# Performance work log

Hardware: AMD Instinct MI355X
Metric: run time of the kernel (lower is better)

Reference implementation:

```python
import jax, jax.numpy as jnp
import numpy as np

NEG_SLOPE = 0.2
LN_EPS = 1e-6

B, L, D, H = 32, 512, 256, 4
N = B * L
E = 65536
C = D  # per-head out channels (GATConv out_channels=d_model)


def setup_inputs() -> dict:
    key = jax.random.key(0)
    ks = jax.random.split(key, 10)
    s = 1.0 / np.sqrt(D)
    inputs = jax.random.normal(ks[0], (B, L, D), dtype=jnp.float32)
    edge_index = jax.random.randint(ks[1], (2, E), 0, N, dtype=jnp.int64)
    return {
        "inputs": inputs,
        "edge_index": edge_index,
        "ln_gamma": jnp.ones((D,), jnp.float32),
        "ln_beta": jnp.zeros((D,), jnp.float32),
        "W1": jax.random.normal(ks[2], (D, D), jnp.float32) * s,   # linear_before_gnn
        "b1": jnp.zeros((D,), jnp.float32),
        "W_gat": jax.random.normal(ks[3], (H * C, D), jnp.float32) * s,  # GATConv.lin (no bias)
        "att_src": jax.random.normal(ks[4], (H, C), jnp.float32) * s,
        "att_dst": jax.random.normal(ks[5], (H, C), jnp.float32) * s,
        "bias_gat": jnp.zeros((C,), jnp.float32),  # concat=False -> size out_channels
        "W2": jax.random.normal(ks[6], (D, D), jnp.float32) * s,   # linear_after_gnn
        "b2": jnp.zeros((D,), jnp.float32),
    }


def _gat_conv(x, edge_index, W_gat, att_src, att_dst, bias_gat):
    # x: [N, D] -> project to [N, H, C]
    xh = (x @ W_gat.T).reshape(N, H, C)
    # add self loops (PyG default add_self_loops=True)
    loops = jnp.arange(N, dtype=edge_index.dtype)
    src = jnp.concatenate([edge_index[0], loops])  # message source j
    dst = jnp.concatenate([edge_index[1], loops])  # message target i
    # per-node attention logits [N, H]
    a_src = jnp.einsum("nhc,hc->nh", xh, att_src)
    a_dst = jnp.einsum("nhc,hc->nh", xh, att_dst)
    # per-edge logits and segment softmax over destination node
    e = jax.nn.leaky_relu(a_src[src] + a_dst[dst], NEG_SLOPE)  # [Etot, H]
    e_max = jax.ops.segment_max(e, dst, num_segments=N)        # every node has a self loop
    e = jnp.exp(e - e_max[dst])
    denom = jax.ops.segment_sum(e, dst, num_segments=N)
    alpha = e / denom[dst]                                     # [Etot, H]
    # weighted message aggregation (dropout on alpha skipped: eval mode)
    msg = xh[src] * alpha[:, :, None]                          # [Etot, H, C]
    out = jax.ops.segment_sum(msg, dst, num_segments=N)        # [N, H, C]
    return out.mean(axis=1) + bias_gat                         # concat=False -> head mean


def reference(inputs, edge_index, ln_gamma, ln_beta, W1, b1, W_gat, att_src, att_dst, bias_gat, W2, b2):
    # LayerNorm(eps=1e-6)
    mu = inputs.mean(-1, keepdims=True)
    var = jnp.mean((inputs - mu) ** 2, axis=-1, keepdims=True)
    x = (inputs - mu) * jax.lax.rsqrt(var + LN_EPS) * ln_gamma + ln_beta
    x = x.reshape(-1, D)
    gnn_in = x @ W1.T + b1
    gnn_out = _gat_conv(gnn_in, edge_index, W_gat, att_src, att_dst, bias_gat)
    y = gnn_out @ W2.T + b2
    # dropout is identity in eval mode; residual add
    return y.reshape(B, L, D) + inputs
```

## Files before the change

### kernel.cpp

```cpp
#include <hip/hip_runtime.h>
#include <math.h>

#define N_NODES 16384
#define D_MODEL 256
#define H_HEADS 4
#define C_CH 256
#define E_EDGES 65536
#define ETOT (E_EDGES + N_NODES)
#define HC 1024

typedef __bf16 bf16x8 __attribute__((ext_vector_type(8)));
typedef __bf16 bf16x4 __attribute__((ext_vector_type(4)));
typedef float f32x4 __attribute__((ext_vector_type(4)));

__device__ __forceinline__ __bf16 f2bf(float f) { return (__bf16)f; }
__device__ __forceinline__ float bf2f(__bf16 b) { return (float)b; }

__global__ __launch_bounds__(256) void prep1_ln(
    const float* __restrict__ Wg, const float* __restrict__ att_src,
    const float* __restrict__ att_dst, const float* __restrict__ W2,
    const int* __restrict__ ei, const float* __restrict__ in,
    const float* __restrict__ gamma, const float* __restrict__ beta,
    float* __restrict__ t, float* __restrict__ V, int* __restrict__ deg,
    __bf16* __restrict__ x_ln)
{
    int b = blockIdx.x;
    int tid = threadIdx.x;
    if (b >= 640) {
        int wave = tid >> 6, lane = tid & 63;
        int row = (b - 640) * 4 + wave;
        float4 v = ((const float4*)(in + (size_t)row * D_MODEL))[lane];
        float s  = v.x + v.y + v.z + v.w;
        float sq = v.x*v.x + v.y*v.y + v.z*v.z + v.w*v.w;
        for (int off = 32; off; off >>= 1) {
            s  += __shfl_xor(s,  off);
            sq += __shfl_xor(sq, off);
        }
        float mean = s * (1.0f / D_MODEL);
        float var  = sq * (1.0f / D_MODEL) - mean * mean;
        float inv  = rsqrtf(var + 1e-6f);
        float4 g = ((const float4*)gamma)[lane];
        float4 bb = ((const float4*)beta)[lane];
        bf16x4 o;
        o[0] = f2bf((v.x - mean) * inv * g.x + bb.x);
        o[1] = f2bf((v.y - mean) * inv * g.y + bb.y);
        o[2] = f2bf((v.z - mean) * inv * g.z + bb.z);
        o[3] = f2bf((v.w - mean) * inv * g.w + bb.w);
        *(bf16x4*)(x_ln + (size_t)row * D_MODEL + lane * 4) = o;
        return;
    }
    if (b < 64) {
        int v = b >> 3, sl = b & 7, h = v & 3;
        const float* att = ((v < 4) ? att_src : att_dst) + h * C_CH;
        float acc = 0.f;
        #pragma unroll
        for (int j = 0; j < 32; ++j) {
            int c = sl * 32 + j;
            acc = fmaf(Wg[(size_t)(h * 256 + c) * 256 + tid], att[c], acc);
        }
        atomicAdd(&t[v * 256 + tid], acc);
    } else if (b < 320) {
        int bb = b - 64;
        int og = (bb & 63) * 4, h = bb >> 6;
        const float* w2r = W2 + (size_t)og * 256;
        const float* wgp = Wg + ((size_t)h * 256) * 256 + tid;
        float a0 = 0.f, a1 = 0.f, a2 = 0.f, a3 = 0.f;
        #pragma unroll 4
        for (int c = 0; c < 256; ++c) {
            float wv = wgp[(size_t)c * 256];
            a0 = fmaf(w2r[c],       wv, a0);
            a1 = fmaf(w2r[256 + c], wv, a1);
            a2 = fmaf(w2r[512 + c], wv, a2);
            a3 = fmaf(w2r[768 + c], wv, a3);
        }
        size_t base = (size_t)og * 1024 + h * 256 + tid;
        V[base]        = a0;
        V[base + 1024] = a1;
        V[base + 2048] = a2;
        V[base + 3072] = a3;
    } else {
        int e = (b - 320) * 256 + tid;
        int dst = (e < E_EDGES) ? ei[E_EDGES + e] : (e - E_EDGES);
        atomicAdd(deg + dst, 1);
    }
}

__global__ __launch_bounds__(256) void prep2(
    const float* __restrict__ t, const float* __restrict__ W1,
    const float* __restrict__ b1, const float* __restrict__ V,
    const float* __restrict__ W2, const float* __restrict__ bg,
    const float* __restrict__ b2, float* __restrict__ u2,
    float* __restrict__ c0, __bf16* __restrict__ Wz,
    float* __restrict__ bias_z, const int* __restrict__ deg,
    int* __restrict__ row_st)
{
    int b = blockIdx.x;
    int d = threadIdx.x;
    if (b < 64) {
        int v = b >> 3, sl = b & 7;
        const float* tv = t + v * 256;
        float acc = 0.f;
        #pragma unroll
        for (int j = 0; j < 32; ++j) {
            int k = sl * 32 + j;
            acc = fmaf(tv[k], W1[(size_t)k * 256 + d], acc);
        }
        atomicAdd(&u2[v * 256 + d], acc);
        if (d < 32) {
            float p = tv[sl * 32 + d] * b1[sl * 32 + d];
            for (int s = 16; s; s >>= 1) p += __shfl_xor(p, s);
            if (d == 0) atomicAdd(&c0[v], p);
        }
        return;
    }
    if (b == 320) {
        __shared__ int wsum[4];
        int lane = d & 63, wid = d >> 6;
        int base = d * 64;
        int run = 0;
        for (int j = 0; j < 64; ++j) run += deg[base + j];
        int x = run;
        #pragma unroll
        for (int off = 1; off < 64; off <<= 1) {
            int y = __shfl_up(x, off);
            if (lane >= off) x += y;
        }
        if (lane == 63) wsum[wid] = x;
        __syncthreads();
        int woff = 0;
        #pragma unroll
        for (int wdx = 0; wdx < 4; ++wdx)
            if (wdx < wid) woff += wsum[wdx];
        int excl = woff + x - run;
        int run2 = 0;
        for (int j = 0; j < 64; ++j) {
            row_st[base + j] = excl + run2;
            run2 += deg[base + j];
        }
        if (d == 255) row_st[N_NODES] = excl + run2;
        return;
    }
    int bb = b - 64;
    int og = (bb & 63) * 4, h = bb >> 6;
    int lane = d & 63, wid = d >> 6;
    const float* vr = V + (size_t)og * 1024 + h * 256;
    float a0 = 0.f, a1 = 0.f, a2 = 0.f, a3 = 0.f;
    #pragma unroll 4
    for (int k = 0; k < 256; ++k) {
        float w1v = W1[(size_t)k * 256 + d];
        a0 = fmaf(vr[k],        w1v, a0);
        a1 = fmaf(vr[1024 + k], w1v, a1);
        a2 = fmaf(vr[2048 + k], w1v, a2);
        a3 = fmaf(vr[3072 + k], w1v, a3);
    }
    size_t base = (size_t)og * 1024 + h * 256 + d;
    Wz[base]        = f2bf(a0);
    Wz[base + 1024] = f2bf(a1);
    Wz[base + 2048] = f2bf(a2);
    Wz[base + 3072] = f2bf(a3);

    __shared__ float red[4][4];
    float b1v = b1[d];
    #pragma unroll
    for (int j = 0; j < 4; ++j) {
        float p = vr[(size_t)j * 1024 + d] * b1v;
        for (int s = 32; s; s >>= 1) p += __shfl_xor(p, s);
        if (lane == 0) red[j][wid] = p;
    }
    __syncthreads();
    if (d < 4) {
        float s = red[d][0] + red[d][1] + red[d][2] + red[d][3];
        atomicAdd(&bias_z[og + d], 0.25f * s);
    }
    if (h == 0) {
        __syncthreads();
        float bgv = bg[d];
        #pragma unroll
        for (int j = 0; j < 4; ++j) {
            float q = W2[(size_t)(og + j) * 256 + d] * bgv;
            for (int s = 32; s; s >>= 1) q += __shfl_xor(q, s);
            if (lane == 0) red[j][wid] = q;
        }
        __syncthreads();
        if (d < 4) {
            float s = red[d][0] + red[d][1] + red[d][2] + red[d][3];
            atomicAdd(&bias_z[og + d], s + b2[og + d]);
        }
    }
}

__global__ __launch_bounds__(256) void logits_scatter(
    const __bf16* __restrict__ x_ln, const float* __restrict__ u2,
    const float* __restrict__ c0, float* __restrict__ a_src,
    float* __restrict__ a_dst, const int* __restrict__ ei,
    const int* __restrict__ row_st, int* __restrict__ cnt,
    int* __restrict__ csr_src)
{
    int b = blockIdx.x;
    int tid = threadIdx.x;
    if (b >= 4096) {
        int e = (b - 4096) * 256 + tid;
        int src, dst;
        if (e < E_EDGES) { src = ei[e]; dst = ei[E_EDGES + e]; }
        else             { src = dst = e - E_EDGES; }
        int pos = atomicAdd(cnt + dst, 1);
        csr_src[row_st[dst] + pos] = src;
        return;
    }
    __shared__ float u2s[8][256];
    __shared__ float c0s[8];
    #pragma unroll
    for (int k = 0; k < 8; ++k) u2s[k][tid] = u2[k * 256 + tid];
    if (tid < 8) c0s[tid] = c0[tid];
    __syncthreads();

    int wave = tid >> 6, lane = tid & 63;
    int n = b * 4 + wave;
    int v = lane >> 3, p = lane & 7;
    const __bf16* xp = x_ln + (size_t)n * D_MODEL + p * 32;
    const float*  up = &u2s[v][p * 32];
    float acc = 0.f;
    #pragma unroll
    for (int ti = 0; ti < 4; ++ti) {
        bf16x8 x = *(const bf16x8*)(xp + ti * 8);
        #pragma unroll
        for (int j = 0; j < 8; ++j)
            acc = fmaf(bf2f(x[j]), up[ti * 8 + j], acc);
    }
    acc += __shfl_xor(acc, 1);
    acc += __shfl_xor(acc, 2);
    acc += __shfl_xor(acc, 4);
    if (p == 0) {
        float o = acc + c0s[v];
        if (v < 4) a_src[n * H_HEADS + v] = o;
        else       a_dst[n * H_HEADS + (v - 4)] = o;
    }
}

__global__ __launch_bounds__(256) void gat_fused(
    const __bf16* __restrict__ x_ln, const float* __restrict__ a_src,
    const float* __restrict__ a_dst, const int* __restrict__ row_start,
    const int* __restrict__ csr_src, __bf16* __restrict__ agg)
{
    int wave = threadIdx.x >> 6, lane = threadIdx.x & 63;
    int i = blockIdx.x * 4 + wave;
    int rs = row_start[i], deg = row_start[i + 1] - rs;
    float4 ad = *(const float4*)(a_dst + i * H_HEADS);

    float acc[4][4] = {};
    float sm0 = 0.f, sm1 = 0.f, sm2 = 0.f, sm3 = 0.f;
    for (int e = 0; e < deg; ++e) {
        int s = csr_src[rs + e];
        float4 as = *(const float4*)(a_src + s * H_HEADS);
        float l0 = as.x + ad.x, l1 = as.y + ad.y, l2 = as.z + ad.z, l3 = as.w + ad.w;
        l0 = (l0 > 0.f) ? l0 : 0.2f * l0;
        l1 = (l1 > 0.f) ? l1 : 0.2f * l1;
        l2 = (l2 > 0.f) ? l2 : 0.2f * l2;
        l3 = (l3 > 0.f) ? l3 : 0.2f * l3;
        float w0 = __expf(l0), w1 = __expf(l1);
        float w2 = __expf(l2), w3 = __expf(l3);
        sm0 += w0; sm1 += w1; sm2 += w2; sm3 += w3;
        bf16x4 x = *(const bf16x4*)(x_ln + (size_t)s * D_MODEL + lane * 4);
        #pragma unroll
        for (int j = 0; j < 4; ++j) {
            float xv = bf2f(x[j]);
            acc[0][j] = fmaf(w0, xv, acc[0][j]);
            acc[1][j] = fmaf(w1, xv, acc[1][j]);
            acc[2][j] = fmaf(w2, xv, acc[2][j]);
            acc[3][j] = fmaf(w3, xv, acc[3][j]);
        }
    }
    float sc[4] = {0.25f / sm0, 0.25f / sm1, 0.25f / sm2, 0.25f / sm3};
    #pragma unroll
    for (int h = 0; h < 4; ++h) {
        bf16x4 o;
        #pragma unroll
        for (int j = 0; j < 4; ++j) o[j] = f2bf(acc[h][j] * sc[h]);
        *(bf16x4*)(agg + (size_t)i * HC + h * 256 + lane * 4) = o;
    }
}

#define APAD 72

__global__ __launch_bounds__(256) void gemm_skinny(
    const __bf16* __restrict__ A, const __bf16* __restrict__ B,
    const float* __restrict__ bias, const float* __restrict__ resid,
    float* __restrict__ outf, int K)
{
    __shared__ __align__(16) __bf16 As[64 * APAD];
    __shared__ __align__(16) __bf16 Bs[256 * APAD];
    int tid  = threadIdx.x;
    int lane = tid & 63;
    int w    = tid >> 6;
    int quad = lane >> 4;
    int l16  = lane & 15;
// ... 79 lines not shown
    for (int nt = 0; nt < 4; ++nt) {
        int col = n0 + nt * 16 + l16;
        float bv = bias[col];
        #pragma unroll
        for (int mt = 0; mt < 4; ++mt) {
            int row = m0 + mt * 16 + quad * 4;
            #pragma unroll
            for (int r = 0; r < 4; ++r) {
                size_t off = (size_t)(row + r) * C_CH + col;
                outf[off] = acc[mt][nt][r] + bv + resid[off];
            }
        }
    }
}

extern "C" void kernel_launch(void* const* d_in, const int* in_sizes, int n_in,
                              void* d_out, int out_size, void* d_ws, size_t ws_size,
                              hipStream_t stream)
{
    const float* inp      = (const float*)d_in[0];
    const int*   ei       = (const int*)  d_in[1];
    const float* ln_gamma = (const float*)d_in[2];
    const float* ln_beta  = (const float*)d_in[3];
    const float* W1       = (const float*)d_in[4];
    const float* b1       = (const float*)d_in[5];
    const float* W_gat    = (const float*)d_in[6];
    const float* att_src  = (const float*)d_in[7];
    const float* att_dst  = (const float*)d_in[8];
    const float* bias_gat = (const float*)d_in[9];
    const float* W2       = (const float*)d_in[10];
    const float* b2       = (const float*)d_in[11];

    char* ws = (char*)d_ws;
    __bf16* x_ln_bf   = (__bf16*)(ws);
    __bf16* agg_bf    = (__bf16*)(ws + (8ull  << 20));
    float*  V_f       = (float*)(ws + (40ull << 20));
    __bf16* Wz_b      = (__bf16*)(ws + (41ull << 20));
    float*  a_src_b   = (float*)(ws + (42ull << 20));
    float*  a_dst_b   = a_src_b + (size_t)N_NODES * H_HEADS;
    float*  t_vec     = a_dst_b + (size_t)N_NODES * H_HEADS;
    float*  u2        = t_vec + 8 * 256;
    float*  c0        = u2 + 8 * 256;
    float*  bias_z    = c0 + 8;
    int*    deg       = (int*)(bias_z + 256);
    int*    cnt       = deg + N_NODES;
    int*    row_st    = cnt + N_NODES;
    int*    csr_src   = row_st + N_NODES + 4;

    size_t zbytes = (8 * 256 + 8 * 256 + 8 + 256) * sizeof(float)
                  + 2 * N_NODES * sizeof(int);
    hipMemsetAsync(t_vec, 0, zbytes, stream);

    prep1_ln<<<640 + 4096, 256, 0, stream>>>(W_gat, att_src, att_dst, W2, ei,
                                             inp, ln_gamma, ln_beta,
                                             t_vec, V_f, deg, x_ln_bf);
    prep2<<<321, 256, 0, stream>>>(t_vec, W1, b1, V_f, W2, bias_gat, b2,
                                   u2, c0, Wz_b, bias_z, deg, row_st);
    logits_scatter<<<4096 + 320, 256, 0, stream>>>(x_ln_bf, u2, c0,
                                                   a_src_b, a_dst_b,
                                                   ei, row_st, cnt, csr_src);
    gat_fused<<<N_NODES / 4, 256, 0, stream>>>(x_ln_bf, a_src_b, a_dst_b,
                                               row_st, csr_src, agg_bf);
    gemm_skinny<<<N_NODES / 64, 256, 0, stream>>>(agg_bf, Wz_b, bias_z, inp,
                                                  (float*)d_out, HC);
}
```

Baseline: 181.8 us.

## Fuse LayerNorm into logits kernel and unroll GAT edge loop by two

LayerNorm moves out of the first prep kernel and into the logits/scatter kernel. The attention logits are now computed from the fp32 normalized values still in registers, so the bf16 x_ln no longer has to be re-read from memory. The per-node GAT aggregation loop is also unrolled by two edges so more gathers are in flight at once. The costs are higher register pressure in gat_fused and slightly different logits, because they now use fp32 instead of bf16-rounded inputs.

```diff
diff --git a/kernel.cpp b/kernel.cpp
--- a/kernel.cpp
+++ b/kernel.cpp
@@ -16,39 +16,14 @@
 __device__ __forceinline__ __bf16 f2bf(float f) { return (__bf16)f; }
 __device__ __forceinline__ float bf2f(__bf16 b) { return (float)b; }
 
-__global__ __launch_bounds__(256) void prep1_ln(
+__global__ __launch_bounds__(256) void prep_w(
     const float* __restrict__ Wg, const float* __restrict__ att_src,
     const float* __restrict__ att_dst, const float* __restrict__ W2,
-    const int* __restrict__ ei, const float* __restrict__ in,
-    const float* __restrict__ gamma, const float* __restrict__ beta,
-    float* __restrict__ t, float* __restrict__ V, int* __restrict__ deg,
-    __bf16* __restrict__ x_ln)
+    const int* __restrict__ ei,
+    float* __restrict__ t, float* __restrict__ V, int* __restrict__ deg)
 {
     int b = blockIdx.x;
     int tid = threadIdx.x;
-    if (b >= 640) {
-        int wave = tid >> 6, lane = tid & 63;
-        int row = (b - 640) * 4 + wave;
-        float4 v = ((const float4*)(in + (size_t)row * D_MODEL))[lane];
-        float s  = v.x + v.y + v.z + v.w;
-        float sq = v.x*v.x + v.y*v.y + v.z*v.z + v.w*v.w;
-        for (int off = 32; off; off >>= 1) {
-            s  += __shfl_xor(s,  off);
-            sq += __shfl_xor(sq, off);
-        }
-        float mean = s * (1.0f / D_MODEL);
-        float var  = sq * (1.0f / D_MODEL) - mean * mean;
-        float inv  = rsqrtf(var + 1e-6f);
-        float4 g = ((const float4*)gamma)[lane];
-        float4 bb = ((const float4*)beta)[lane];
-        bf16x4 o;
-        o[0] = f2bf((v.x - mean) * inv * g.x + bb.x);
-        o[1] = f2bf((v.y - mean) * inv * g.y + bb.y);
-        o[2] = f2bf((v.z - mean) * inv * g.z + bb.z);
-        o[3] = f2bf((v.w - mean) * inv * g.w + bb.w);
-        *(bf16x4*)(x_ln + (size_t)row * D_MODEL + lane * 4) = o;
-        return;
-    }
     if (b < 64) {
         int v = b >> 3, sl = b & 7, h = v & 3;
         const float* att = ((v < 4) ? att_src : att_dst) + h * C_CH;
@@ -189,12 +164,13 @@
     }
 }
 
-__global__ __launch_bounds__(256) void logits_scatter(
-    const __bf16* __restrict__ x_ln, const float* __restrict__ u2,
-    const float* __restrict__ c0, float* __restrict__ a_src,
-    float* __restrict__ a_dst, const int* __restrict__ ei,
-    const int* __restrict__ row_st, int* __restrict__ cnt,
-    int* __restrict__ csr_src)
+__global__ __launch_bounds__(256) void ln_logits_scatter(
+    const float* __restrict__ in, const float* __restrict__ gamma,
+    const float* __restrict__ beta, const float* __restrict__ u2,
+    const float* __restrict__ c0, __bf16* __restrict__ x_ln,
+    float* __restrict__ a_src, float* __restrict__ a_dst,
+    const int* __restrict__ ei, const int* __restrict__ row_st,
+    int* __restrict__ cnt, int* __restrict__ csr_src)
 {
     int b = blockIdx.x;
     int tid = threadIdx.x;
@@ -207,7 +183,7 @@
         csr_src[row_st[dst] + pos] = src;
         return;
     }
-    __shared__ float u2s[8][256];
+    __shared__ __align__(16) float u2s[8][256];
     __shared__ float c0s[8];
     #pragma unroll
     for (int k = 0; k < 8; ++k) u2s[k][tid] = u2[k * 256 + tid];
@@ -215,25 +191,38 @@
     __syncthreads();
 
     int wave = tid >> 6, lane = tid & 63;
-    int n = b * 4 + wave;
-    int v = lane >> 3, p = lane & 7;
-    const __bf16* xp = x_ln + (size_t)n * D_MODEL + p * 32;
-    const float*  up = &u2s[v][p * 32];
-    float acc = 0.f;
-    #pragma unroll
-    for (int ti = 0; ti < 4; ++ti) {
-        bf16x8 x = *(const bf16x8*)(xp + ti * 8);
-        #pragma unroll
-        for (int j = 0; j < 8; ++j)
-            acc = fmaf(bf2f(x[j]), up[ti * 8 + j], acc);
-    }
-    acc += __shfl_xor(acc, 1);
-    acc += __shfl_xor(acc, 2);
-    acc += __shfl_xor(acc, 4);
-    if (p == 0) {
-        float o = acc + c0s[v];
-        if (v < 4) a_src[n * H_HEADS + v] = o;
-        else       a_dst[n * H_HEADS + (v - 4)] = o;
+    int row = b * 4 + wave;
+    float4 v = ((const float4*)(in + (size_t)row * D_MODEL))[lane];
+    float s  = v.x + v.y + v.z + v.w;
+    float sq = v.x*v.x + v.y*v.y + v.z*v.z + v.w*v.w;
+    for (int off = 32; off; off >>= 1) {
+        s  += __shfl_xor(s,  off);
+        sq += __shfl_xor(sq, off);
+    }
+    float mean = s * (1.0f / D_MODEL);
+    float var  = sq * (1.0f / D_MODEL) - mean * mean;
+    float inv  = rsqrtf(var + 1e-6f);
+    float4 g  = ((const float4*)gamma)[lane];
+    float4 bb = ((const float4*)beta)[lane];
+    float xr0 = (v.x - mean) * inv * g.x + bb.x;
+    float xr1 = (v.y - mean) * inv * g.y + bb.y;
+    float xr2 = (v.z - mean) * inv * g.z + bb.z;
+    float xr3 = (v.w - mean) * inv * g.w + bb.w;
+    bf16x4 o;
+    o[0] = f2bf(xr0); o[1] = f2bf(xr1); o[2] = f2bf(xr2); o[3] = f2bf(xr3);
+    *(bf16x4*)(x_ln + (size_t)row * D_MODEL + lane * 4) = o;
+
+    #pragma unroll
+    for (int vv = 0; vv < 8; ++vv) {
+        float4 u = *(const float4*)&u2s[vv][lane * 4];
+        float p = xr0 * u.x + xr1 * u.y + xr2 * u.z + xr3 * u.w;
+        #pragma unroll
+        for (int off = 32; off; off >>= 1) p += __shfl_xor(p, off);
+        if (lane == 0) {
+            float oo = p + c0s[vv];
+            if (vv < 4) a_src[row * H_HEADS + vv] = oo;
+            else        a_dst[row * H_HEADS + (vv - 4)] = oo;
+        }
     }
 }
 
@@ -249,10 +238,52 @@
 
     float acc[4][4] = {};
     float sm0 = 0.f, sm1 = 0.f, sm2 = 0.f, sm3 = 0.f;
-    for (int e = 0; e < deg; ++e) {
+    int e = 0;
+    for (; e + 2 <= deg; e += 2) {
+        int s0 = csr_src[rs + e];
+        int s1 = csr_src[rs + e + 1];
+        float4 as0 = *(const float4*)(a_src + s0 * H_HEADS);
+        float4 as1 = *(const float4*)(a_src + s1 * H_HEADS);
+        bf16x4 x0 = *(const bf16x4*)(x_ln + (size_t)s0 * D_MODEL + lane * 4);
+        bf16x4 x1 = *(const bf16x4*)(x_ln + (size_t)s1 * D_MODEL + lane * 4);
+        float l00 = as0.x + ad.x, l01 = as0.y + ad.y,
+              l02 = as0.z + ad.z, l03 = as0.w + ad.w;
+        float l10 = as1.x + ad.x, l11 = as1.y + ad.y,
+              l12 = as1.z + ad.z, l13 = as1.w + ad.w;
+        l00 = (l00 > 0.f) ? l00 : 0.2f * l00;
+        l01 = (l01 > 0.f) ? l01 : 0.2f * l01;
+        l02 = (l02 > 0.f) ? l02 : 0.2f * l02;
+        l03 = (l03 > 0.f) ? l03 : 0.2f * l03;
+        l10 = (l10 > 0.f) ? l10 : 0.2f * l10;
+        l11 = (l11 > 0.f) ? l11 : 0.2f * l11;
+        l12 = (l12 > 0.f) ? l12 : 0.2f * l12;
+        l13 = (l13 > 0.f) ? l13 : 0.2f * l13;
+        float w00 = __expf(l00), w01 = __expf(l01),
+              w02 = __expf(l02), w03 = __expf(l03);
+        float w10 = __expf(l10), w11 = __expf(l11),
+              w12 = __expf(l12), w13 = __expf(l13);
+        sm0 += w00 + w10; sm1 += w01 + w11;
+        sm2 += w02 + w12; sm3 += w03 + w13;
+        #pragma unroll
+        for (int j = 0; j < 4; ++j) {
+            float xv0 = bf2f(x0[j]);
+            float xv1 = bf2f(x1[j]);
+            acc[0][j] = fmaf(w00, xv0, acc[0][j]);
+            acc[1][j] = fmaf(w01, xv0, acc[1][j]);
+            acc[2][j] = fmaf(w02, xv0, acc[2][j]);
+            acc[3][j] = fmaf(w03, xv0, acc[3][j]);
+            acc[0][j] = fmaf(w10, xv1, acc[0][j]);
+            acc[1][j] = fmaf(w11, xv1, acc[1][j]);
+            acc[2][j] = fmaf(w12, xv1, acc[2][j]);
+            acc[3][j] = fmaf(w13, xv1, acc[3][j]);
+        }
+    }
+    if (e < deg) {
         int s = csr_src[rs + e];
         float4 as = *(const float4*)(a_src + s * H_HEADS);
-        float l0 = as.x + ad.x, l1 = as.y + ad.y, l2 = as.z + ad.z, l3 = as.w + ad.w;
+        bf16x4 x = *(const bf16x4*)(x_ln + (size_t)s * D_MODEL + lane * 4);
+        float l0 = as.x + ad.x, l1 = as.y + ad.y,
+              l2 = as.z + ad.z, l3 = as.w + ad.w;
         l0 = (l0 > 0.f) ? l0 : 0.2f * l0;
         l1 = (l1 > 0.f) ? l1 : 0.2f * l1;
         l2 = (l2 > 0.f) ? l2 : 0.2f * l2;
@@ -260,7 +291,6 @@
         float w0 = __expf(l0), w1 = __expf(l1);
         float w2 = __expf(l2), w3 = __expf(l3);
         sm0 += w0; sm1 += w1; sm2 += w2; sm3 += w3;
-        bf16x4 x = *(const bf16x4*)(x_ln + (size_t)s * D_MODEL + lane * 4);
         #pragma unroll
         for (int j = 0; j < 4; ++j) {
             float xv = bf2f(x[j]);
@@ -425,14 +455,14 @@
                   + 2 * N_NODES * sizeof(int);
     hipMemsetAsync(t_vec, 0, zbytes, stream);
 
-    prep1_ln<<<640 + 4096, 256, 0, stream>>>(W_gat, att_src, att_dst, W2, ei,
-                                             inp, ln_gamma, ln_beta,
-                                             t_vec, V_f, deg, x_ln_bf);
+    prep_w<<<640, 256, 0, stream>>>(W_gat, att_src, att_dst, W2, ei,
+                                    t_vec, V_f, deg);
     prep2<<<321, 256, 0, stream>>>(t_vec, W1, b1, V_f, W2, bias_gat, b2,
                                    u2, c0, Wz_b, bias_z, deg, row_st);
-    logits_scatter<<<4096 + 320, 256, 0, stream>>>(x_ln_bf, u2, c0,
-                                                   a_src_b, a_dst_b,
-                                                   ei, row_st, cnt, csr_src);
+    ln_logits_scatter<<<4096 + 320, 256, 0, stream>>>(inp, ln_gamma, ln_beta,
+                                                      u2, c0, x_ln_bf,
+                                                      a_src_b, a_dst_b,
+                                                      ei, row_st, cnt, csr_src);
     gat_fused<<<N_NODES / 4, 256, 0, stream>>>(x_ln_bf, a_src_b, a_dst_b,
                                                row_st, csr_src, agg_bf);
     gemm_skinny<<<N_NODES / 64, 256, 0, stream>>>(agg_bf, Wz_b, bias_z, inp,
```

Result: no change. 184.2 us (+1.3%).

## Merge prep kernels, use fixed-slot adjacency buckets, unroll GAT edge loop

Applied to the files above, without the earlier changes.

Folds the two prep kernels into one launch. A single block now computes the attention-projected vectors and u2/c0 serially instead of through atomics, and the other blocks compute the fused W2·Wg·W1 weights through shared memory. The degree count and prefix scan are replaced by fixed-capacity per-node buckets of 64 slots filled by atomic counters. The GAT kernel loads each node's source list once per lane and shuffles it to every lane, with a 4-way unrolled edge loop that overlaps the gathers. This removes kernel launches and the serial scan, but silently assumes no node has an in-degree above 64, and the single-block prep step may become a serial tail.

```diff
diff --git a/kernel.cpp b/kernel.cpp
--- a/kernel.cpp
+++ b/kernel.cpp
@@ -8,6 +8,7 @@
 #define E_EDGES 65536
 #define ETOT (E_EDGES + N_NODES)
 #define HC 1024
+#define MAXDEG 64
 
 typedef __bf16 bf16x8 __attribute__((ext_vector_type(8)));
 typedef __bf16 bf16x4 __attribute__((ext_vector_type(4)));
@@ -16,19 +17,23 @@
 __device__ __forceinline__ __bf16 f2bf(float f) { return (__bf16)f; }
 __device__ __forceinline__ float bf2f(__bf16 b) { return (float)b; }
 
-__global__ __launch_bounds__(256) void prep1_ln(
+__global__ __launch_bounds__(256) void fused_prep_ln(
     const float* __restrict__ Wg, const float* __restrict__ att_src,
-    const float* __restrict__ att_dst, const float* __restrict__ W2,
+    const float* __restrict__ att_dst, const float* __restrict__ W1,
+    const float* __restrict__ b1, const float* __restrict__ W2,
+    const float* __restrict__ bg, const float* __restrict__ b2,
     const int* __restrict__ ei, const float* __restrict__ in,
     const float* __restrict__ gamma, const float* __restrict__ beta,
-    float* __restrict__ t, float* __restrict__ V, int* __restrict__ deg,
-    __bf16* __restrict__ x_ln)
+    __bf16* __restrict__ x_ln, __bf16* __restrict__ Wz,
+    float* __restrict__ bias_z, float* __restrict__ u2,
+    float* __restrict__ c0, int* __restrict__ cnt, int* __restrict__ csr)
 {
     int b = blockIdx.x;
     int tid = threadIdx.x;
-    if (b >= 640) {
+
+    if (b >= 577) {
         int wave = tid >> 6, lane = tid & 63;
-        int row = (b - 640) * 4 + wave;
+        int row = (b - 577) * 4 + wave;
         float4 v = ((const float4*)(in + (size_t)row * D_MODEL))[lane];
         float s  = v.x + v.y + v.z + v.w;
         float sq = v.x*v.x + v.y*v.y + v.z*v.z + v.w*v.w;
@@ -39,7 +44,7 @@
         float mean = s * (1.0f / D_MODEL);
         float var  = sq * (1.0f / D_MODEL) - mean * mean;
         float inv  = rsqrtf(var + 1e-6f);
-        float4 g = ((const float4*)gamma)[lane];
+        float4 g  = ((const float4*)gamma)[lane];
         float4 bb = ((const float4*)beta)[lane];
         bf16x4 o;
         o[0] = f2bf((v.x - mean) * inv * g.x + bb.x);
@@ -49,19 +54,49 @@
         *(bf16x4*)(x_ln + (size_t)row * D_MODEL + lane * 4) = o;
         return;
     }
-    if (b < 64) {
-        int v = b >> 3, sl = b & 7, h = v & 3;
-        const float* att = ((v < 4) ? att_src : att_dst) + h * C_CH;
-        float acc = 0.f;
-        #pragma unroll
-        for (int j = 0; j < 32; ++j) {
-            int c = sl * 32 + j;
-            acc = fmaf(Wg[(size_t)(h * 256 + c) * 256 + tid], att[c], acc);
-        }
-        atomicAdd(&t[v * 256 + tid], acc);
-    } else if (b < 320) {
-        int bb = b - 64;
+
+    if (b == 0) {
+        __shared__ float tsh[8][256];
+        float tv[8] = {0.f, 0.f, 0.f, 0.f, 0.f, 0.f, 0.f, 0.f};
+        #pragma unroll
+        for (int h = 0; h < 4; ++h) {
+            const float* as = att_src + h * 256;
+            const float* ad = att_dst + h * 256;
+            const float* wcol = Wg + ((size_t)h * 256) * 256 + tid;
+            #pragma unroll 4
+            for (int c = 0; c < 256; ++c) {
+                float wv = wcol[(size_t)c * 256];
+                tv[h]     = fmaf(wv, as[c], tv[h]);
+                tv[h + 4] = fmaf(wv, ad[c], tv[h + 4]);
+            }
+        }
+        #pragma unroll
+        for (int v = 0; v < 8; ++v) tsh[v][tid] = tv[v];
+        __syncthreads();
+        float u[8] = {0.f, 0.f, 0.f, 0.f, 0.f, 0.f, 0.f, 0.f};
+        #pragma unroll 4
+        for (int k = 0; k < 256; ++k) {
+            float w1v = W1[(size_t)k * 256 + tid];
+            #pragma unroll
+            for (int v = 0; v < 8; ++v) u[v] = fmaf(tsh[v][k], w1v, u[v]);
+        }
+        #pragma unroll
+        for (int v = 0; v < 8; ++v) u2[v * 256 + tid] = u[v];
+        if (tid < 8) {
+            float s = 0.f;
+            for (int k = 0; k < 256; ++k) s = fmaf(tsh[tid][k], b1[k], s);
+            c0[tid] = s;
+        }
+        return;
+    }
+
+    if (b < 257) {
+        int bb = b - 1;
         int og = (bb & 63) * 4, h = bb >> 6;
+        int lane = tid & 63, wid = tid >> 6;
+        __shared__ float vsh[4][256];
+        __shared__ float red[4][4];
+
         const float* w2r = W2 + (size_t)og * 256;
         const float* wgp = Wg + ((size_t)h * 256) * 256 + tid;
         float a0 = 0.f, a1 = 0.f, a2 = 0.f, a3 = 0.f;
@@ -73,140 +108,71 @@
             a2 = fmaf(w2r[512 + c], wv, a2);
             a3 = fmaf(w2r[768 + c], wv, a3);
         }
+        vsh[0][tid] = a0; vsh[1][tid] = a1; vsh[2][tid] = a2; vsh[3][tid] = a3;
+        __syncthreads();
+
+        float o0 = 0.f, o1 = 0.f, o2 = 0.f, o3 = 0.f;
+        #pragma unroll 4
+        for (int k = 0; k < 256; ++k) {
+            float w1v = W1[(size_t)k * 256 + tid];
+            o0 = fmaf(vsh[0][k], w1v, o0);
+            o1 = fmaf(vsh[1][k], w1v, o1);
+            o2 = fmaf(vsh[2][k], w1v, o2);
+            o3 = fmaf(vsh[3][k], w1v, o3);
+        }
         size_t base = (size_t)og * 1024 + h * 256 + tid;
-        V[base]        = a0;
-        V[base + 1024] = a1;
-        V[base + 2048] = a2;
-        V[base + 3072] = a3;
-    } else {
-        int e = (b - 320) * 256 + tid;
-        int dst = (e < E_EDGES) ? ei[E_EDGES + e] : (e - E_EDGES);
-        atomicAdd(deg + dst, 1);
-    }
-}
-
-__global__ __launch_bounds__(256) void prep2(
-    const float* __restrict__ t, const float* __restrict__ W1,
-    const float* __restrict__ b1, const float* __restrict__ V,
-    const float* __restrict__ W2, const float* __restrict__ bg,
-    const float* __restrict__ b2, float* __restrict__ u2,
-    float* __restrict__ c0, __bf16* __restrict__ Wz,
-    float* __restrict__ bias_z, const int* __restrict__ deg,
-    int* __restrict__ row_st)
-{
-    int b = blockIdx.x;
-    int d = threadIdx.x;
-    if (b < 64) {
-        int v = b >> 3, sl = b & 7;
-        const float* tv = t + v * 256;
-        float acc = 0.f;
-        #pragma unroll
-        for (int j = 0; j < 32; ++j) {
-            int k = sl * 32 + j;
-            acc = fmaf(tv[k], W1[(size_t)k * 256 + d], acc);
-        }
-        atomicAdd(&u2[v * 256 + d], acc);
-        if (d < 32) {
-            float p = tv[sl * 32 + d] * b1[sl * 32 + d];
-            for (int s = 16; s; s >>= 1) p += __shfl_xor(p, s);
-            if (d == 0) atomicAdd(&c0[v], p);
+        Wz[base]        = f2bf(o0);
+        Wz[base + 1024] = f2bf(o1);
+        Wz[base + 2048] = f2bf(o2);
+        Wz[base + 3072] = f2bf(o3);
+
+        float b1v = b1[tid];
+        #pragma unroll
+        for (int j = 0; j < 4; ++j) {
+            float p = vsh[j][tid] * b1v;
+            for (int s = 32; s; s >>= 1) p += __shfl_xor(p, s);
+            if (lane == 0) red[j][wid] = p;
+        }
+        __syncthreads();
+        if (tid < 4) {
+            float s = red[tid][0] + red[tid][1] + red[tid][2] + red[tid][3];
+            atomicAdd(&bias_z[og + tid], 0.25f * s);
+        }
+        if (h == 0) {
+            __syncthreads();
+            float bgv = bg[tid];
+            #pragma unroll
+            for (int j = 0; j < 4; ++j) {
+                float q = W2[(size_t)(og + j) * 256 + tid] * bgv;
+                for (int s = 32; s; s >>= 1) q += __shfl_xor(q, s);
+                if (lane == 0) red[j][wid] = q;
+            }
+            __syncthreads();
+            if (tid < 4) {
+                float s = red[tid][0] + red[tid][1] + red[tid][2] + red[tid][3];
+                atomicAdd(&bias_z[og + tid], s + b2[og + tid]);
+            }
         }
         return;
     }
-    if (b == 320) {
-        __shared__ int wsum[4];
-        int lane = d & 63, wid = d >> 6;
-        int base = d * 64;
-        int run = 0;
-        for (int j = 0; j < 64; ++j) run += deg[base + j];
-        int x = run;
-        #pragma unroll
-        for (int off = 1; off < 64; off <<= 1) {
-            int y = __shfl_up(x, off);
-            if (lane >= off) x += y;
-        }
-        if (lane == 63) wsum[wid] = x;
-        __syncthreads();
-        int woff = 0;
-        #pragma unroll
-        for (int wdx = 0; wdx < 4; ++wdx)
-            if (wdx < wid) woff += wsum[wdx];
-        int excl = woff + x - run;
-        int run2 = 0;
-        for (int j = 0; j < 64; ++j) {
-            row_st[base + j] = excl + run2;
-            run2 += deg[base + j];
-        }
-        if (d == 255) row_st[N_NODES] = excl + run2;
-        return;
-    }
-    int bb = b - 64;
-    int og = (bb & 63) * 4, h = bb >> 6;
-    int lane = d & 63, wid = d >> 6;
-    const float* vr = V + (size_t)og * 1024 + h * 256;
-    float a0 = 0.f, a1 = 0.f, a2 = 0.f, a3 = 0.f;
-    #pragma unroll 4
-    for (int k = 0; k < 256; ++k) {
-        float w1v = W1[(size_t)k * 256 + d];
-        a0 = fmaf(vr[k],        w1v, a0);
-        a1 = fmaf(vr[1024 + k], w1v, a1);
-        a2 = fmaf(vr[2048 + k], w1v, a2);
-        a3 = fmaf(vr[3072 + k], w1v, a3);
-    }
-    size_t base = (size_t)og * 1024 + h * 256 + d;
-    Wz[base]        = f2bf(a0);
-    Wz[base + 1024] = f2bf(a1);
-    Wz[base + 2048] = f2bf(a2);
-    Wz[base + 3072] = f2bf(a3);
-
-    __shared__ float red[4][4];
-    float b1v = b1[d];
-    #pragma unroll
-    for (int j = 0; j < 4; ++j) {
-        float p = vr[(size_t)j * 1024 + d] * b1v;
-        for (int s = 32; s; s >>= 1) p += __shfl_xor(p, s);
-        if (lane == 0) red[j][wid] = p;
-    }
-    __syncthreads();
-    if (d < 4) {
-        float s = red[d][0] + red[d][1] + red[d][2] + red[d][3];
-        atomicAdd(&bias_z[og + d], 0.25f * s);
-    }
-    if (h == 0) {
-        __syncthreads();
-        float bgv = bg[d];
-        #pragma unroll
-        for (int j = 0; j < 4; ++j) {
-            float q = W2[(size_t)(og + j) * 256 + d] * bgv;
-            for (int s = 32; s; s >>= 1) q += __shfl_xor(q, s);
-            if (lane == 0) red[j][wid] = q;
-        }
-        __syncthreads();
-        if (d < 4) {
-            float s = red[d][0] + red[d][1] + red[d][2] + red[d][3];
-            atomicAdd(&bias_z[og + d], s + b2[og + d]);
-        }
-    }
-}
-
-__global__ __launch_bounds__(256) void logits_scatter(
-    const __bf16* __restrict__ x_ln, const float* __restrict__ u2,
-    const float* __restrict__ c0, float* __restrict__ a_src,
-    float* __restrict__ a_dst, const int* __restrict__ ei,
-    const int* __restrict__ row_st, int* __restrict__ cnt,
-    int* __restrict__ csr_src)
-{
-    int b = blockIdx.x;
-    int tid = threadIdx.x;
-    if (b >= 4096) {
-        int e = (b - 4096) * 256 + tid;
+
+    {
+        int e = (b - 257) * 256 + tid;
         int src, dst;
         if (e < E_EDGES) { src = ei[e]; dst = ei[E_EDGES + e]; }
         else             { src = dst = e - E_EDGES; }
         int pos = atomicAdd(cnt + dst, 1);
-        csr_src[row_st[dst] + pos] = src;
-        return;
-    }
+        csr[(size_t)dst * MAXDEG + pos] = src;
+    }
+}
+
+__global__ __launch_bounds__(256) void logits_k(
+    const __bf16* __restrict__ x_ln, const float* __restrict__ u2,
+    const float* __restrict__ c0, float* __restrict__ a_src,
+    float* __restrict__ a_dst)
+{
+    int b = blockIdx.x;
+    int tid = threadIdx.x;
     __shared__ float u2s[8][256];
     __shared__ float c0s[8];
     #pragma unroll
@@ -239,20 +205,72 @@
 
 __global__ __launch_bounds__(256) void gat_fused(
     const __bf16* __restrict__ x_ln, const float* __restrict__ a_src,
-    const float* __restrict__ a_dst, const int* __restrict__ row_start,
-    const int* __restrict__ csr_src, __bf16* __restrict__ agg)
+    const float* __restrict__ a_dst, const int* __restrict__ cnt,
+    const int* __restrict__ csr, __bf16* __restrict__ agg)
 {
     int wave = threadIdx.x >> 6, lane = threadIdx.x & 63;
     int i = blockIdx.x * 4 + wave;
-    int rs = row_start[i], deg = row_start[i + 1] - rs;
+    int deg = cnt[i];
+    int sidx = csr[(size_t)i * MAXDEG + lane];
     float4 ad = *(const float4*)(a_dst + i * H_HEADS);
 
     float acc[4][4] = {};
     float sm0 = 0.f, sm1 = 0.f, sm2 = 0.f, sm3 = 0.f;
-    for (int e = 0; e < deg; ++e) {
-        int s = csr_src[rs + e];
+
+    int e = 0;
+    for (; e + 4 <= deg; e += 4) {
+        int s0 = __shfl(sidx, e);
+        int s1 = __shfl(sidx, e + 1);
+        int s2 = __shfl(sidx, e + 2);
+        int s3 = __shfl(sidx, e + 3);
+        float4 A0 = *(const float4*)(a_src + s0 * H_HEADS);
+        float4 A1 = *(const float4*)(a_src + s1 * H_HEADS);
+        float4 A2 = *(const float4*)(a_src + s2 * H_HEADS);
+        float4 A3 = *(const float4*)(a_src + s3 * H_HEADS);
+        bf16x4 X0 = *(const bf16x4*)(x_ln + (size_t)s0 * D_MODEL + lane * 4);
+        bf16x4 X1 = *(const bf16x4*)(x_ln + (size_t)s1 * D_MODEL + lane * 4);
+        bf16x4 X2 = *(const bf16x4*)(x_ln + (size_t)s2 * D_MODEL + lane * 4);
+        bf16x4 X3 = *(const bf16x4*)(x_ln + (size_t)s3 * D_MODEL + lane * 4);
+
+        float l[4][4] = {
+            {A0.x + ad.x, A0.y + ad.y, A0.z + ad.z, A0.w + ad.w},
+            {A1.x + ad.x, A1.y + ad.y, A1.z + ad.z, A1.w + ad.w},
+            {A2.x + ad.x, A2.y + ad.y, A2.z + ad.z, A2.w + ad.w},
+            {A3.x + ad.x, A3.y + ad.y, A3.z + ad.z, A3.w + ad.w}};
+        float wgt[4][4];
+        #pragma unroll
+        for (int q = 0; q < 4; ++q)
+            #pragma unroll
+            for (int h = 0; h < 4; ++h) {
+                float lv = l[q][h];
+                lv = (lv > 0.f) ? lv : 0.2f * lv;
+                wgt[q][h] = __expf(lv);
+            }
+        sm0 += wgt[0][0] + wgt[1][0] + wgt[2][0] + wgt[3][0];
+        sm1 += wgt[0][1] + wgt[1][1] + wgt[2][1] + wgt[3][1];
+        sm2 += wgt[0][2] + wgt[1][2] + wgt[2][2] + wgt[3][2];
+        sm3 += wgt[0][3] + wgt[1][3] + wgt[2][3] + wgt[3][3];
+        #pragma unroll
+        for (int j = 0; j < 4; ++j) {
+            float x0 = bf2f(X0[j]), x1 = bf2f(X1[j]);
+            float x2 = bf2f(X2[j]), x3 = bf2f(X3[j]);
+            #pragma unroll
+            for (int h = 0; h < 4; ++h) {
+                float a = acc[h][j];
+                a = fmaf(wgt[0][h], x0, a);
+                a = fmaf(wgt[1][h], x1, a);
+                a = fmaf(wgt[2][h], x2, a);
+                a = fmaf(wgt[3][h], x3, a);
+                acc[h][j] = a;
+            }
+        }
+    }
+    for (; e < deg; ++e) {
+        int s = __shfl(sidx, e);
         float4 as = *(const float4*)(a_src + s * H_HEADS);
-        float l0 = as.x + ad.x, l1 = as.y + ad.y, l2 = as.z + ad.z, l3 = as.w + ad.w;
+        bf16x4 x = *(const bf16x4*)(x_ln + (size_t)s * D_MODEL + lane * 4);
+        float l0 = as.x + ad.x, l1 = as.y + ad.y,
+              l2 = as.z + ad.z, l3 = as.w + ad.w;
         l0 = (l0 > 0.f) ? l0 : 0.2f * l0;
         l1 = (l1 > 0.f) ? l1 : 0.2f * l1;
         l2 = (l2 > 0.f) ? l2 : 0.2f * l2;
@@ -260,7 +278,6 @@
         float w0 = __expf(l0), w1 = __expf(l1);
         float w2 = __expf(l2), w3 = __expf(l3);
         sm0 += w0; sm1 += w1; sm2 += w2; sm3 += w3;
-        bf16x4 x = *(const bf16x4*)(x_ln + (size_t)s * D_MODEL + lane * 4);
         #pragma unroll
         for (int j = 0; j < 4; ++j) {
             float xv = bf2f(x[j]);
@@ -406,35 +423,27 @@
     const float* b2       = (const float*)d_in[11];
 
     char* ws = (char*)d_ws;
-    __bf16* x_ln_bf   = (__bf16*)(ws);
-    __bf16* agg_bf    = (__bf16*)(ws + (8ull  << 20));
-    float*  V_f       = (float*)(ws + (40ull << 20));
-    __bf16* Wz_b      = (__bf16*)(ws + (41ull << 20));
-    float*  a_src_b   = (float*)(ws + (42ull << 20));
-    float*  a_dst_b   = a_src_b + (size_t)N_NODES * H_HEADS;
-    float*  t_vec     = a_dst_b + (size_t)N_NODES * H_HEADS;
-    float*  u2        = t_vec + 8 * 256;
-    float*  c0        = u2 + 8 * 256;
-    float*  bias_z    = c0 + 8;
-    int*    deg       = (int*)(bias_z + 256);
-    int*    cnt       = deg + N_NODES;
-    int*    row_st    = cnt + N_NODES;
-    int*    csr_src   = row_st + N_NODES + 4;
-
-    size_t zbytes = (8 * 256 + 8 * 256 + 8 + 256) * sizeof(float)
-                  + 2 * N_NODES * sizeof(int);
-    hipMemsetAsync(t_vec, 0, zbytes, stream);
-
-    prep1_ln<<<640 + 4096, 256, 0, stream>>>(W_gat, att_src, att_dst, W2, ei,
-                                             inp, ln_gamma, ln_beta,
-                                             t_vec, V_f, deg, x_ln_bf);
-    prep2<<<321, 256, 0, stream>>>(t_vec, W1, b1, V_f, W2, bias_gat, b2,
-                                   u2, c0, Wz_b, bias_z, deg, row_st);
-    logits_scatter<<<4096 + 320, 256, 0, stream>>>(x_ln_bf, u2, c0,
-                                                   a_src_b, a_dst_b,
-                                                   ei, row_st, cnt, csr_src);
+    __bf16* x_ln_bf = (__bf16*)(ws);
+    __bf16* agg_bf  = (__bf16*)(ws + (8ull  << 20));
+    __bf16* Wz_b    = (__bf16*)(ws + (40ull << 20));
+    float*  a_src_b = (float*)(ws + (41ull << 20));
+    float*  a_dst_b = a_src_b + (size_t)N_NODES * H_HEADS;
+    float*  u2      = (float*)(ws + (42ull << 20));
+    float*  c0      = u2 + 8 * 256;
+    float*  bias_z  = c0 + 8;
+    int*    cnt     = (int*)(bias_z + 256);
+    int*    csr     = (int*)(ws + (43ull << 20));
+
+    size_t zbytes = 256 * sizeof(float) + N_NODES * sizeof(int);
+    hipMemsetAsync(bias_z, 0, zbytes, stream);
+
+    fused_prep_ln<<<577 + 4096, 256, 0, stream>>>(
+        W_gat, att_src, att_dst, W1, b1, W2, bias_gat, b2, ei,
+        inp, ln_gamma, ln_beta, x_ln_bf, Wz_b, bias_z, u2, c0, cnt, csr);
+    logits_k<<<N_NODES / 4, 256, 0, stream>>>(x_ln_bf, u2, c0,
+                                              a_src_b, a_dst_b);
     gat_fused<<<N_NODES / 4, 256, 0, stream>>>(x_ln_bf, a_src_b, a_dst_b,
-                                               row_st, csr_src, agg_bf);
+                                               cnt, csr, agg_bf);
     gemm_skinny<<<N_NODES / 64, 256, 0, stream>>>(agg_bf, Wz_b, bias_z, inp,
                                                   (float*)d_out, HC);
 }
```

Result: slower. 204.5 us (+12.5%).

## Split-K weight-fold GEMVs with atomics, vectorize prefix scan, unroll GAT edge loop

Applied to the files above, without the earlier changes.

The W2·Wgat and V·W1 weight-folding products are now split four ways along the reduction dimension, giving four times as many blocks, with partial sums combined through float atomics into a zeroed fp32 buffer. A new block range in the logits kernel converts that buffer to bf16. The degree prefix scan now uses int4 vector loads and stores, and the GAT aggregation loop processes two edges per iteration so the gathers can be in flight together. The cost is extra memset bytes, atomic traffic, and run-to-run nondeterministic float summation order.

```diff
diff --git a/kernel.cpp b/kernel.cpp
--- a/kernel.cpp
+++ b/kernel.cpp
@@ -26,9 +26,9 @@
 {
     int b = blockIdx.x;
     int tid = threadIdx.x;
-    if (b >= 640) {
+    if (b >= 1408) {
         int wave = tid >> 6, lane = tid & 63;
-        int row = (b - 640) * 4 + wave;
+        int row = (b - 1408) * 4 + wave;
         float4 v = ((const float4*)(in + (size_t)row * D_MODEL))[lane];
         float s  = v.x + v.y + v.z + v.w;
         float sq = v.x*v.x + v.y*v.y + v.z*v.z + v.w*v.w;
@@ -59,14 +59,18 @@
             acc = fmaf(Wg[(size_t)(h * 256 + c) * 256 + tid], att[c], acc);
         }
         atomicAdd(&t[v * 256 + tid], acc);
-    } else if (b < 320) {
-        int bb = b - 64;
-        int og = (bb & 63) * 4, h = bb >> 6;
+        return;
+    }
+    if (b < 1088) {
+        int bb2 = b - 64;
+        int orig = bb2 >> 2, cs = bb2 & 3;
+        int og = (orig & 63) * 4, h = orig >> 6;
         const float* w2r = W2 + (size_t)og * 256;
         const float* wgp = Wg + ((size_t)h * 256) * 256 + tid;
         float a0 = 0.f, a1 = 0.f, a2 = 0.f, a3 = 0.f;
+        int cb = cs * 64;
         #pragma unroll 4
-        for (int c = 0; c < 256; ++c) {
+        for (int c = cb; c < cb + 64; ++c) {
             float wv = wgp[(size_t)c * 256];
             a0 = fmaf(w2r[c],       wv, a0);
             a1 = fmaf(w2r[256 + c], wv, a1);
@@ -74,12 +78,14 @@
             a3 = fmaf(w2r[768 + c], wv, a3);
         }
         size_t base = (size_t)og * 1024 + h * 256 + tid;
-        V[base]        = a0;
-        V[base + 1024] = a1;
-        V[base + 2048] = a2;
-        V[base + 3072] = a3;
-    } else {
-        int e = (b - 320) * 256 + tid;
+        atomicAdd(&V[base],        a0);
+        atomicAdd(&V[base + 1024], a1);
+        atomicAdd(&V[base + 2048], a2);
+        atomicAdd(&V[base + 3072], a3);
+        return;
+    }
+    {
+        int e = (b - 1088) * 256 + tid;
         int dst = (e < E_EDGES) ? ei[E_EDGES + e] : (e - E_EDGES);
         atomicAdd(deg + dst, 1);
     }
@@ -90,14 +96,70 @@
     const float* __restrict__ b1, const float* __restrict__ V,
     const float* __restrict__ W2, const float* __restrict__ bg,
     const float* __restrict__ b2, float* __restrict__ u2,
-    float* __restrict__ c0, __bf16* __restrict__ Wz,
+    float* __restrict__ c0, float* __restrict__ Wzf,
     float* __restrict__ bias_z, const int* __restrict__ deg,
     int* __restrict__ row_st)
 {
+    __shared__ float red[4][4];
+    __shared__ int wsum[4];
     int b = blockIdx.x;
     int d = threadIdx.x;
-    if (b < 64) {
-        int v = b >> 3, sl = b & 7;
+
+    if (b < 1024) {
+        int orig = b >> 2, ks = b & 3;
+        int og = (orig & 63) * 4, h = orig >> 6;
+        int lane = d & 63, wid = d >> 6;
+        const float* vr = V + (size_t)og * 1024 + h * 256;
+        float a0 = 0.f, a1 = 0.f, a2 = 0.f, a3 = 0.f;
+        int kb = ks * 64;
+        #pragma unroll 4
+        for (int k = kb; k < kb + 64; ++k) {
+            float w1v = W1[(size_t)k * 256 + d];
+            a0 = fmaf(vr[k],        w1v, a0);
+            a1 = fmaf(vr[1024 + k], w1v, a1);
+            a2 = fmaf(vr[2048 + k], w1v, a2);
+            a3 = fmaf(vr[3072 + k], w1v, a3);
+        }
+        size_t base = (size_t)og * 1024 + h * 256 + d;
+        atomicAdd(&Wzf[base],        a0);
+        atomicAdd(&Wzf[base + 1024], a1);
+        atomicAdd(&Wzf[base + 2048], a2);
+        atomicAdd(&Wzf[base + 3072], a3);
+
+        if (ks == 0) {
+            float b1v = b1[d];
+            #pragma unroll
+            for (int j = 0; j < 4; ++j) {
+                float p = vr[(size_t)j * 1024 + d] * b1v;
+                for (int s = 32; s; s >>= 1) p += __shfl_xor(p, s);
+                if (lane == 0) red[j][wid] = p;
+            }
+            __syncthreads();
+            if (d < 4) {
+                float s = red[d][0] + red[d][1] + red[d][2] + red[d][3];
+                atomicAdd(&bias_z[og + d], 0.25f * s);
+            }
+            if (h == 0) {
+                __syncthreads();
+                float bgv = bg[d];
+                #pragma unroll
+                for (int j = 0; j < 4; ++j) {
+                    float q = W2[(size_t)(og + j) * 256 + d] * bgv;
+                    for (int s = 32; s; s >>= 1) q += __shfl_xor(q, s);
+                    if (lane == 0) red[j][wid] = q;
+                }
+                __syncthreads();
+                if (d < 4) {
+                    float s = red[d][0] + red[d][1] + red[d][2] + red[d][3];
+                    atomicAdd(&bias_z[og + d], s + b2[og + d]);
+                }
+            }
+        }
+        return;
+    }
+    if (b < 1088) {
+        int bb = b - 1024;
+        int v = bb >> 3, sl = bb & 7;
         const float* tv = t + v * 256;
         float acc = 0.f;
         #pragma unroll
@@ -113,12 +175,16 @@
         }
         return;
     }
-    if (b == 320) {
-        __shared__ int wsum[4];
+    {
         int lane = d & 63, wid = d >> 6;
         int base = d * 64;
+        int4 dv[16];
+        #pragma unroll
+        for (int j = 0; j < 16; ++j) dv[j] = ((const int4*)(deg + base))[j];
         int run = 0;
-        for (int j = 0; j < 64; ++j) run += deg[base + j];
+        #pragma unroll
+        for (int j = 0; j < 16; ++j)
+            run += dv[j].x + dv[j].y + dv[j].z + dv[j].w;
         int x = run;
         #pragma unroll
         for (int off = 1; off < 64; off <<= 1) {
@@ -132,72 +198,38 @@
         for (int wdx = 0; wdx < 4; ++wdx)
             if (wdx < wid) woff += wsum[wdx];
         int excl = woff + x - run;
-        int run2 = 0;
-        for (int j = 0; j < 64; ++j) {
-            row_st[base + j] = excl + run2;
-            run2 += deg[base + j];
-        }
-        if (d == 255) row_st[N_NODES] = excl + run2;
-        return;
-    }
-    int bb = b - 64;
-    int og = (bb & 63) * 4, h = bb >> 6;
-    int lane = d & 63, wid = d >> 6;
-    const float* vr = V + (size_t)og * 1024 + h * 256;
-    float a0 = 0.f, a1 = 0.f, a2 = 0.f, a3 = 0.f;
-    #pragma unroll 4
-    for (int k = 0; k < 256; ++k) {
-        float w1v = W1[(size_t)k * 256 + d];
-        a0 = fmaf(vr[k],        w1v, a0);
-        a1 = fmaf(vr[1024 + k], w1v, a1);
-        a2 = fmaf(vr[2048 + k], w1v, a2);
-        a3 = fmaf(vr[3072 + k], w1v, a3);
-    }
-    size_t base = (size_t)og * 1024 + h * 256 + d;
-    Wz[base]        = f2bf(a0);
-    Wz[base + 1024] = f2bf(a1);
-    Wz[base + 2048] = f2bf(a2);
-    Wz[base + 3072] = f2bf(a3);
-
-    __shared__ float red[4][4];
-    float b1v = b1[d];
-    #pragma unroll
-    for (int j = 0; j < 4; ++j) {
-        float p = vr[(size_t)j * 1024 + d] * b1v;
-        for (int s = 32; s; s >>= 1) p += __shfl_xor(p, s);
-        if (lane == 0) red[j][wid] = p;
-    }
-    __syncthreads();
-    if (d < 4) {
-        float s = red[d][0] + red[d][1] + red[d][2] + red[d][3];
-        atomicAdd(&bias_z[og + d], 0.25f * s);
-    }
-    if (h == 0) {
-        __syncthreads();
-        float bgv = bg[d];
-        #pragma unroll
-        for (int j = 0; j < 4; ++j) {
-            float q = W2[(size_t)(og + j) * 256 + d] * bgv;
-            for (int s = 32; s; s >>= 1) q += __shfl_xor(q, s);
-            if (lane == 0) red[j][wid] = q;
-        }
-        __syncthreads();
-        if (d < 4) {
-            float s = red[d][0] + red[d][1] + red[d][2] + red[d][3];
-            atomicAdd(&bias_z[og + d], s + b2[og + d]);
-        }
+        int r2v = 0;
+        #pragma unroll
+        for (int j = 0; j < 16; ++j) {
+            int4 w;
+            w.x = excl + r2v; r2v += dv[j].x;
+            w.y = excl + r2v; r2v += dv[j].y;
+            w.z = excl + r2v; r2v += dv[j].z;
+            w.w = excl + r2v; r2v += dv[j].w;
+            ((int4*)(row_st + base))[j] = w;
+        }
+        if (d == 255) row_st[N_NODES] = excl + r2v;
     }
 }
 
-__global__ __launch_bounds__(256) void logits_scatter(
+__global__ __launch_bounds__(256) void logits_scatter_cvt(
     const __bf16* __restrict__ x_ln, const float* __restrict__ u2,
     const float* __restrict__ c0, float* __restrict__ a_src,
     float* __restrict__ a_dst, const int* __restrict__ ei,
     const int* __restrict__ row_st, int* __restrict__ cnt,
-    int* __restrict__ csr_src)
+    int* __restrict__ csr_src, const float* __restrict__ Wzf,
+    __bf16* __restrict__ Wz)
 {
     int b = blockIdx.x;
     int tid = threadIdx.x;
+    if (b >= 4416) {
+        int idx = (b - 4416) * 256 + tid;
+        float4 v = ((const float4*)Wzf)[idx];
+        bf16x4 o;
+        o[0] = f2bf(v.x); o[1] = f2bf(v.y); o[2] = f2bf(v.z); o[3] = f2bf(v.w);
+        *(bf16x4*)(Wz + (size_t)idx * 4) = o;
+        return;
+    }
     if (b >= 4096) {
         int e = (b - 4096) * 256 + tid;
         int src, dst;
@@ -249,10 +281,52 @@
 
     float acc[4][4] = {};
     float sm0 = 0.f, sm1 = 0.f, sm2 = 0.f, sm3 = 0.f;
-    for (int e = 0; e < deg; ++e) {
+    int e = 0;
+    for (; e + 2 <= deg; e += 2) {
+        int s0 = csr_src[rs + e];
+        int s1 = csr_src[rs + e + 1];
+        float4 as0 = *(const float4*)(a_src + s0 * H_HEADS);
+        float4 as1 = *(const float4*)(a_src + s1 * H_HEADS);
+        bf16x4 x0 = *(const bf16x4*)(x_ln + (size_t)s0 * D_MODEL + lane * 4);
+        bf16x4 x1 = *(const bf16x4*)(x_ln + (size_t)s1 * D_MODEL + lane * 4);
+        float l00 = as0.x + ad.x, l01 = as0.y + ad.y,
+              l02 = as0.z + ad.z, l03 = as0.w + ad.w;
+        float l10 = as1.x + ad.x, l11 = as1.y + ad.y,
+              l12 = as1.z + ad.z, l13 = as1.w + ad.w;
+        l00 = (l00 > 0.f) ? l00 : 0.2f * l00;
+        l01 = (l01 > 0.f) ? l01 : 0.2f * l01;
+        l02 = (l02 > 0.f) ? l02 : 0.2f * l02;
+        l03 = (l03 > 0.f) ? l03 : 0.2f * l03;
+        l10 = (l10 > 0.f) ? l10 : 0.2f * l10;
+        l11 = (l11 > 0.f) ? l11 : 0.2f * l11;
+        l12 = (l12 > 0.f) ? l12 : 0.2f * l12;
+        l13 = (l13 > 0.f) ? l13 : 0.2f * l13;
+        float w00 = __expf(l00), w01 = __expf(l01),
+              w02 = __expf(l02), w03 = __expf(l03);
+        float w10 = __expf(l10), w11 = __expf(l11),
+              w12 = __expf(l12), w13 = __expf(l13);
+        sm0 += w00 + w10; sm1 += w01 + w11;
+        sm2 += w02 + w12; sm3 += w03 + w13;
+        #pragma unroll
+        for (int j = 0; j < 4; ++j) {
+            float xv0 = bf2f(x0[j]);
+            float xv1 = bf2f(x1[j]);
+            acc[0][j] = fmaf(w00, xv0, acc[0][j]);
+            acc[1][j] = fmaf(w01, xv0, acc[1][j]);
+            acc[2][j] = fmaf(w02, xv0, acc[2][j]);
+            acc[3][j] = fmaf(w03, xv0, acc[3][j]);
+            acc[0][j] = fmaf(w10, xv1, acc[0][j]);
+            acc[1][j] = fmaf(w11, xv1, acc[1][j]);
+            acc[2][j] = fmaf(w12, xv1, acc[2][j]);
+            acc[3][j] = fmaf(w13, xv1, acc[3][j]);
+        }
+    }
+    if (e < deg) {
         int s = csr_src[rs + e];
         float4 as = *(const float4*)(a_src + s * H_HEADS);
-        float l0 = as.x + ad.x, l1 = as.y + ad.y, l2 = as.z + ad.z, l3 = as.w + ad.w;
+        bf16x4 x = *(const bf16x4*)(x_ln + (size_t)s * D_MODEL + lane * 4);
+        float l0 = as.x + ad.x, l1 = as.y + ad.y,
+              l2 = as.z + ad.z, l3 = as.w + ad.w;
         l0 = (l0 > 0.f) ? l0 : 0.2f * l0;
         l1 = (l1 > 0.f) ? l1 : 0.2f * l1;
         l2 = (l2 > 0.f) ? l2 : 0.2f * l2;
@@ -260,7 +334,6 @@
         float w0 = __expf(l0), w1 = __expf(l1);
         float w2 = __expf(l2), w3 = __expf(l3);
         sm0 += w0; sm1 += w1; sm2 += w2; sm3 += w3;
-        bf16x4 x = *(const bf16x4*)(x_ln + (size_t)s * D_MODEL + lane * 4);
         #pragma unroll
         for (int j = 0; j < 4; ++j) {
             float xv = bf2f(x[j]);
@@ -406,33 +479,35 @@
     const float* b2       = (const float*)d_in[11];
 
     char* ws = (char*)d_ws;
-    __bf16* x_ln_bf   = (__bf16*)(ws);
-    __bf16* agg_bf    = (__bf16*)(ws + (8ull  << 20));
-    float*  V_f       = (float*)(ws + (40ull << 20));
-    __bf16* Wz_b      = (__bf16*)(ws + (41ull << 20));
-    float*  a_src_b   = (float*)(ws + (42ull << 20));
-    float*  a_dst_b   = a_src_b + (size_t)N_NODES * H_HEADS;
-    float*  t_vec     = a_dst_b + (size_t)N_NODES * H_HEADS;
-    float*  u2        = t_vec + 8 * 256;
-    float*  c0        = u2 + 8 * 256;
-    float*  bias_z    = c0 + 8;
-    int*    deg       = (int*)(bias_z + 256);
-    int*    cnt       = deg + N_NODES;
-    int*    row_st    = cnt + N_NODES;
-    int*    csr_src   = row_st + N_NODES + 4;
-
-    size_t zbytes = (8 * 256 + 8 * 256 + 8 + 256) * sizeof(float)
-                  + 2 * N_NODES * sizeof(int);
+    __bf16* x_ln_bf = (__bf16*)(ws);
+    __bf16* agg_bf  = (__bf16*)(ws + (8ull  << 20));
+    __bf16* Wz_b    = (__bf16*)(ws + (40ull << 20));
+    float*  a_src_b = (float*)(ws + (41ull << 20));
+    float*  a_dst_b = a_src_b + (size_t)N_NODES * H_HEADS;
+    float*  t_vec   = (float*)(ws + (42ull << 20));
+    float*  u2      = t_vec + 2048;
+    float*  c0      = u2 + 2048;
+    float*  bias_z  = c0 + 8;
+    int*    deg     = (int*)(bias_z + 256);
+    int*    cnt     = deg + N_NODES;
+    float*  V_f     = (float*)(cnt + N_NODES);
+    float*  Wzf     = V_f + 256 * 1024;
+    int*    row_st  = (int*)(Wzf + 256 * 1024);
+    int*    csr_src = row_st + N_NODES + 4;
+
+    size_t zbytes = (2048 + 2048 + 8 + 256) * sizeof(float)
+                  + 2 * N_NODES * sizeof(int)
+                  + 2 * 256 * 1024 * sizeof(float);
     hipMemsetAsync(t_vec, 0, zbytes, stream);
 
-    prep1_ln<<<640 + 4096, 256, 0, stream>>>(W_gat, att_src, att_dst, W2, ei,
-                                             inp, ln_gamma, ln_beta,
-                                             t_vec, V_f, deg, x_ln_bf);
-    prep2<<<321, 256, 0, stream>>>(t_vec, W1, b1, V_f, W2, bias_gat, b2,
-                                   u2, c0, Wz_b, bias_z, deg, row_st);
-    logits_scatter<<<4096 + 320, 256, 0, stream>>>(x_ln_bf, u2, c0,
-                                                   a_src_b, a_dst_b,
-                                                   ei, row_st, cnt, csr_src);
+    prep1_ln<<<1408 + 4096, 256, 0, stream>>>(W_gat, att_src, att_dst, W2, ei,
+                                              inp, ln_gamma, ln_beta,
+                                              t_vec, V_f, deg, x_ln_bf);
+    prep2<<<1089, 256, 0, stream>>>(t_vec, W1, b1, V_f, W2, bias_gat, b2,
+                                    u2, c0, Wzf, bias_z, deg, row_st);
+    logits_scatter_cvt<<<4096 + 320 + 256, 256, 0, stream>>>(
+        x_ln_bf, u2, c0, a_src_b, a_dst_b, ei, row_st, cnt, csr_src,
+        Wzf, Wz_b);
     gat_fused<<<N_NODES / 4, 256, 0, stream>>>(x_ln_bf, a_src_b, a_dst_b,
                                                row_st, csr_src, agg_bf);
     gemm_skinny<<<N_NODES / 64, 256, 0, stream>>>(agg_bf, Wz_b, bias_z, inp,
```

Measured after the change: 165.2 us. -9.1%, faster.
